# Optimization experiments

Measured on AMD Instinct MI355X. Metric: run time of the kernel, lower is better.

The kernel has to match this reference:

```python
import jax, jax.numpy as jnp
import numpy as np


def _hungarian(cost):
    """Jonker-Volgenant shortest-augmenting-path LAP solver (minimum cost).

    Returns col_ind such that rows arange(n) are matched to columns col_ind,
    identical (in objective) to scipy.optimize.linear_sum_assignment.
    Runs on host numpy, mirroring the original's detach().cpu() + scipy path.
    """
    cost = np.asarray(cost, dtype=np.float64)
    n = cost.shape[0]
    INF = np.inf
    u = np.zeros(n + 1)
    v = np.zeros(n + 1)
    p = np.zeros(n + 1, dtype=np.int64)   # p[j]: row (1-based) assigned to column j
    way = np.zeros(n + 1, dtype=np.int64)
    for i in range(1, n + 1):
        p[0] = i
        j0 = 0
        minv = np.full(n + 1, INF)
        used = np.zeros(n + 1, dtype=bool)
        while True:
            used[j0] = True
            i0 = p[j0]
            # vectorized relaxation of reduced costs for all unused columns
            cur = cost[i0 - 1] - u[i0] - v[1:]
            free = ~used[1:]
            upd = free & (cur < minv[1:])
            minv[1:] = np.where(upd, cur, minv[1:])
            way[1:] = np.where(upd, j0, way[1:])
            cand = np.where(free, minv[1:], INF)
            j1 = int(np.argmin(cand)) + 1
            delta = cand[j1 - 1]
            u[p[used]] += delta
            v[used] -= delta
            minv[1:] = np.where(free, minv[1:] - delta, minv[1:])
            j0 = j1
            if p[j0] == 0:
                break
        # augment along the alternating path
        while j0:
            j1 = way[j0]
            p[j0] = p[j1]
            j0 = j1
    col = np.empty(n, dtype=np.int64)
    col[p[1:] - 1] = np.arange(n)
    return col


def setup_inputs() -> dict:
    key = jax.random.key(0)
    B, N = 64, 256
    D = jax.random.normal(key, (B, N, N), dtype=jnp.float32)
    return {"D": D}


def reference(D):
    # Host round-trip for the assignment, exactly as the torch module does
    # (D.detach().cpu().numpy() -> scipy LAP per batch element).
    Dn = np.asarray(jax.device_get(D))
    cols = np.stack([_hungarian(Dn[b]) for b in range(Dn.shape[0])])  # [B, N]
    idx = jnp.asarray(cols)[:, :, None]                               # [B, N, 1]
    # gather matched costs D[b, i, col[b, i]] and reduce: mean per batch, then mean
    matched = jnp.take_along_axis(D, idx, axis=2)[..., 0]             # [B, N]
    return matched.mean(axis=1).mean()
```

## Files before the change

### kernel.cpp

```cpp
#include <hip/hip_runtime.h>

#define N_DIM 256
#define BATCH 64
#define BS 64
#define SCALE 4096.0f

#define DPP_MINU(x, ctrl) do {                                                 \
    unsigned _s = (unsigned)__builtin_amdgcn_update_dpp((int)(x), (int)(x),    \
                                                        (ctrl), 0xf, 0xf, false); \
    (x) = ((x) < _s) ? (x) : _s;                                               \
} while (0)

__device__ __forceinline__ unsigned wave_min_u32(unsigned x) {
    DPP_MINU(x, 0x111);
    DPP_MINU(x, 0x112);
    DPP_MINU(x, 0x114);
    DPP_MINU(x, 0x118);
    const unsigned a = (unsigned)__builtin_amdgcn_readlane((int)x, 15);
    const unsigned b = (unsigned)__builtin_amdgcn_readlane((int)x, 31);
    const unsigned c = (unsigned)__builtin_amdgcn_readlane((int)x, 47);
    const unsigned d = (unsigned)__builtin_amdgcn_readlane((int)x, 63);
    const unsigned ab = (a < b) ? a : b;
    const unsigned cd = (c < d) ? c : d;
    return (ab < cd) ? ab : cd;
}

__device__ __forceinline__ int rd4_i(int x0, int x1, int x2, int x3, int idx) {
    const int sel = idx & 3, src = idx >> 2;
    int ab = (sel & 1) ? x1 : x0;
    int cd = (sel & 1) ? x3 : x2;
    int vv = (sel & 2) ? cd : ab;
    return __builtin_amdgcn_readlane(vv, src);
}

#define SET4(x0, x1, x2, x3, idx, val) do {                                    \
    const int _sel = (idx) & 3;                                                \
    if (t == ((idx) >> 2)) {                                                   \
        if (_sel == 0) x0 = (val); else if (_sel == 1) x1 = (val);             \
        else if (_sel == 2) x2 = (val); else x3 = (val);                       \
    }                                                                          \
} while (0)

__device__ __forceinline__ int lo16(int p) { return (int)(short)(p & 0xFFFF); }
__device__ __forceinline__ int hi16(int p) { return p >> 16; }

__global__ __launch_bounds__(BS) void lap_kernel(const float* __restrict__ Dm,
                                                 double* __restrict__ batch_sums) {
    const int b = blockIdx.x;
    const int t = threadIdx.x;
    const float* __restrict__ cost = Dm + (size_t)b * N_DIM * N_DIM;
    const float4* __restrict__ cost4 = (const float4*)cost;

    __shared__ int2     chi[N_DIM * BS];
    __shared__ int      u_s[N_DIM];
    __shared__ int      v_s[N_DIM];
    __shared__ int      row4col_s[N_DIM];
    __shared__ int      col4row_s[N_DIM];
    __shared__ int      queue_s[N_DIM];
    __shared__ unsigned bid_s[N_DIM];
    __shared__ int      qcnt_s;

    const int c0i = 4 * t, c1i = 4 * t + 1, c2i = 4 * t + 2, c3i = 4 * t + 3;

    int cmn0 = INT_MAX, cmn1 = INT_MAX, cmn2 = INT_MAX, cmn3 = INT_MAX;
    int ca0 = 0, ca1 = 0, ca2 = 0, ca3 = 0;
    for (int r = 0; r < N_DIM; ++r) {
        const float4 c4 = cost4[r * BS + t];
        const int a0 = __float2int_rn(c4.x * SCALE);
        const int a1 = __float2int_rn(c4.y * SCALE);
        const int a2 = __float2int_rn(c4.z * SCALE);
        const int a3 = __float2int_rn(c4.w * SCALE);
        int2 p;
        p.x = (a0 & 0xFFFF) | (a1 << 16);
        p.y = (a2 & 0xFFFF) | (a3 << 16);
        chi[r * BS + t] = p;
        if (a0 < cmn0) { cmn0 = a0; ca0 = r; }
        if (a1 < cmn1) { cmn1 = a1; ca1 = r; }
        if (a2 < cmn2) { cmn2 = a2; ca2 = r; }
        if (a3 < cmn3) { cmn3 = a3; ca3 = r; }
    }
    {
        int4 vv; vv.x = cmn0; vv.y = cmn1; vv.z = cmn2; vv.w = cmn3;
        ((int4*)v_s)[t] = vv;
        int4 zz; zz.x = 0; zz.y = 0; zz.z = 0; zz.w = 0;
        ((int4*)u_s)[t] = zz;
        int4 mm; mm.x = -1; mm.y = -1; mm.z = -1; mm.w = -1;
        ((int4*)row4col_s)[t] = mm;
        ((int4*)col4row_s)[t] = mm;
        int4 rc; rc.x = 0x7fffffff; rc.y = 0x7fffffff; rc.z = 0x7fffffff; rc.w = 0x7fffffff;
        ((int4*)queue_s)[t] = rc;
        uint4 bb; bb.x = ~0u; bb.y = ~0u; bb.z = ~0u; bb.w = ~0u;
        ((uint4*)bid_s)[t] = bb;
    }
    __syncthreads();
    atomicMin(&queue_s[ca0], c0i);
    atomicMin(&queue_s[ca1], c1i);
    atomicMin(&queue_s[ca2], c2i);
    atomicMin(&queue_s[ca3], c3i);
    __syncthreads();
    if (queue_s[ca0] == c0i) { row4col_s[c0i] = ca0; col4row_s[ca0] = c0i; }
    if (queue_s[ca1] == c1i) { row4col_s[c1i] = ca1; col4row_s[ca1] = c1i; }
    if (queue_s[ca2] == c2i) { row4col_s[c2i] = ca2; col4row_s[ca2] = c2i; }
    if (queue_s[ca3] == c3i) { row4col_s[c3i] = ca3; col4row_s[ca3] = c3i; }
    __syncthreads();

    for (int pass = 0; pass < 24; ++pass) {
        if (t == 0) qcnt_s = 0;
        __syncthreads();
        {
            const int4 my = ((const int4*)col4row_s)[t];
            const int nf = (my.x < 0) + (my.y < 0) + (my.z < 0) + (my.w < 0);
            if (nf) {
                int pos = atomicAdd(&qcnt_s, nf);
                if (my.x < 0) queue_s[pos++] = c0i;
                if (my.y < 0) queue_s[pos++] = c1i;
                if (my.z < 0) queue_s[pos++] = c2i;
                if (my.w < 0) queue_s[pos++] = c3i;
            }
        }
        __syncthreads();
        const int n = qcnt_s;
        if (n == 0) break;
        for (int base = 0; base < n; base += BS) {
            const int my_row = (base + t < n) ? queue_s[base + t] : -1;
            int d1 = INT_MAX, d2 = INT_MAX;
            int j1 = 0;
            if (my_row >= 0) {
                const int rb = my_row * BS;
                for (int l = 0; l < BS; ++l) {
                    const int l2 = (l + t) & 63;
                    const int2 h = chi[rb + l2];
                    const int4 vv = ((const int4*)v_s)[l2];
                    int d;
                    d = lo16(h.x) - vv.x; if (d < d1) { d2 = d1; d1 = d; j1 = 4 * l2 + 0; } else if (d < d2) d2 = d;
                    d = hi16(h.x) - vv.y; if (d < d1) { d2 = d1; d1 = d; j1 = 4 * l2 + 1; } else if (d < d2) d2 = d;
                    d = lo16(h.y) - vv.z; if (d < d1) { d2 = d1; d1 = d; j1 = 4 * l2 + 2; } else if (d < d2) d2 = d;
                    d = hi16(h.y) - vv.w; if (d < d1) { d2 = d1; d1 = d; j1 = 4 * l2 + 3; } else if (d < d2) d2 = d;
                }
                atomicMin(&bid_s[j1], ((unsigned)d1 << 8) | (unsigned)t);
            }
            __syncthreads();
            if (my_row >= 0) {
                const unsigned mybid = ((unsigned)d1 << 8) | (unsigned)t;
                if (bid_s[j1] == mybid) {
                    const int i0 = row4col_s[j1];
                    row4col_s[j1] = my_row;
                    col4row_s[my_row] = j1;
                    if (i0 >= 0) col4row_s[i0] = -1;
                    u_s[my_row] = d2;
                    v_s[j1] += d1 - d2;
                    bid_s[j1] = ~0u;
                }
            }
            __syncthreads();
        }
    }

    const int4 vv4 = ((const int4*)v_s)[t];
    int vn0 = -vv4.x, vn1 = -vv4.y, vn2 = -vv4.z, vn3 = -vv4.w;
    const int4 m4 = ((const int4*)row4col_s)[t];
    int r4c0 = m4.x, r4c1 = m4.y, r4c2 = m4.z, r4c3 = m4.w;
    const int4 y4 = ((const int4*)col4row_s)[t];
    int c4r0 = y4.x, c4r1 = y4.y, c4r2 = y4.z, c4r3 = y4.w;
    int p0 = 0, p1 = 0, p2 = 0, p3 = 0;

    unsigned long long fm0 = __ballot(c4r0 < 0);
    unsigned long long fm1 = __ballot(c4r1 < 0);
    unsigned long long fm2 = __ballot(c4r2 < 0);
    unsigned long long fm3 = __ballot(c4r3 < 0);

    const int KINIT0 = (0x7FFFFF << 8) | c0i;
    const int KINIT1 = (0x7FFFFF << 8) | c1i;
    const int KINIT2 = (0x7FFFFF << 8) | c2i;
    const int KINIT3 = (0x7FFFFF << 8) | c3i;

    while (fm0 | fm1 | fm2 | fm3) {
        int i;
        if (fm0)      { const int tt = __builtin_ctzll(fm0); fm0 &= fm0 - 1; i = tt * 4 + 0; }
        else if (fm1) { const int tt = __builtin_ctzll(fm1); fm1 &= fm1 - 1; i = tt * 4 + 1; }
        else if (fm2) { const int tt = __builtin_ctzll(fm2); fm2 &= fm2 - 1; i = tt * 4 + 2; }
        else          { const int tt = __builtin_ctzll(fm3); fm3 &= fm3 - 1; i = tt * 4 + 3; }

        int k0 = KINIT0, k1 = KINIT1, k2 = KINIT2, k3 = KINIT3;
        int g0 = 0, g1 = 0, g2 = 0, g3 = 0;
        int cur = i;
        int minVal = 0;
        int sink = -1;

        while (true) {
            const int2 h   = chi[cur * BS + t];
            const int ucur = u_s[cur];
            const int add  = minVal - ucur;

            int r, kn;
            r  = add + lo16(h.x) + vn0;
            kn = (r << 8) | c0i; if (kn < k0) { p0 = cur; k0 = kn; }
            r  = add + hi16(h.x) + vn1;
            kn = (r << 8) | c1i; if (kn < k1) { p1 = cur; k1 = kn; }
            r  = add + lo16(h.y) + vn2;
            kn = (r << 8) | c2i; if (kn < k2) { p2 = cur; k2 = kn; }
            r  = add + hi16(h.y) + vn3;
            kn = (r << 8) | c3i; if (kn < k3) { p3 = cur; k3 = kn; }

            const int q0 = k0 | g0, q1 = k1 | g1, q2 = k2 | g2, q3 = k3 | g3;
            int q01 = (q0 < q1) ? q0 : q1;
            int q23 = (q2 < q3) ? q2 : q3;
            const int gk = (int)wave_min_u32((unsigned)((q01 < q23) ? q01 : q23));

            const int bi = gk & 0xFF;
            minVal = gk >> 8;
            const int r4 = rd4_i(r4c0, r4c1, r4c2, r4c3, bi);
            if (t == (bi >> 2)) {
                const int s = bi & 3;
                if (s == 0) g0 = 0x7FFFFFFF; else if (s == 1) g1 = 0x7FFFFFFF;
                else if (s == 2) g2 = 0x7FFFFFFF; else g3 = 0x7FFFFFFF;
            }
            if (r4 < 0) { sink = bi; break; }
            cur = r4;
        }

        if (g0) { const int dv = minVal - (k0 >> 8); vn0 += dv; if (r4c0 >= 0) u_s[r4c0] += dv; }
        if (g1) { const int dv = minVal - (k1 >> 8); vn1 += dv; if (r4c1 >= 0) u_s[r4c1] += dv; }
        if (g2) { const int dv = minVal - (k2 >> 8); vn2 += dv; if (r4c2 >= 0) u_s[r4c2] += dv; }
        if (g3) { const int dv = minVal - (k3 >> 8); vn3 += dv; if (r4c3 >= 0) u_s[r4c3] += dv; }
        if (t == 0) u_s[i] += minVal;

        if (sink >= 0) {
            int jj = sink;
            while (true) {
                const int ii = rd4_i(p0, p1, p2, p3, jj);
                SET4(r4c0, r4c1, r4c2, r4c3, jj, ii);
                const int tmp = rd4_i(c4r0, c4r1, c4r2, c4r3, ii);
                SET4(c4r0, c4r1, c4r2, c4r3, ii, jj);
                jj = tmp;
                if (ii == i) break;
            }
        }
    }

    double s = 0.0;
    s += (double)cost[(size_t)(t * 4 + 0) * N_DIM + c4r0];
    s += (double)cost[(size_t)(t * 4 + 1) * N_DIM + c4r1];
    s += (double)cost[(size_t)(t * 4 + 2) * N_DIM + c4r2];
    s += (double)cost[(size_t)(t * 4 + 3) * N_DIM + c4r3];
    #pragma unroll
    for (int off = 32; off > 0; off >>= 1) s += __shfl_down(s, off);
    if (t == 0) batch_sums[b] = s;
}

__global__ void finalize_kernel(const double* __restrict__ batch_sums,
                                float* __restrict__ out) {
    const int t = threadIdx.x;
    double s = batch_sums[t];
    #pragma unroll
    for (int off = 32; off > 0; off >>= 1) s += __shfl_down(s, off);
    if (t == 0) out[0] = (float)(s / (double)((long long)BATCH * N_DIM));
}

extern "C" void kernel_launch(void* const* d_in, const int* in_sizes, int n_in,
                              void* d_out, int out_size, void* d_ws, size_t ws_size,
                              hipStream_t stream) {
    const float* Dm = (const float*)d_in[0];
    float* out = (float*)d_out;
    double* sums = (double*)d_ws;

    lap_kernel<<<BATCH, BS, 0, stream>>>(Dm, sums);
    finalize_kernel<<<1, 64, 0, stream>>>(sums, out);
}
```

Before: 725.8 us.

## Speculatively prefetch next Dijkstra row in LAP shortest-path loop and halve auction passes

Restructures the shortest-augmenting-path inner loop to speculate on the second-best column. It prefetches that column's cost row and dual before relaxing the current row, then commits the speculative step only if the relaxation did not produce a smaller key anywhere in the wave. This is meant to hide LDS load latency and the serial dependency of the wave-min reduction. It also halves the number of initial auction/greedy passes, which leaves more rows for the slower exact phase. The speculation adds an extra wave reduction and ballot per iteration, and mis-speculation wastes loads.

```diff
diff --git a/kernel.cpp b/kernel.cpp
--- a/kernel.cpp
+++ b/kernel.cpp
@@ -39,6 +39,26 @@
         if (_sel == 0) x0 = (val); else if (_sel == 1) x1 = (val);             \
         else if (_sel == 2) x2 = (val); else x3 = (val);                       \
     }                                                                          \
+} while (0)
+
+#define SET_GUARD(idx) do {                                                    \
+    if (t == ((idx) >> 2)) {                                                   \
+        const int _s = (idx) & 3;                                              \
+        if (_s == 0) g0 = 0x7FFFFFFF; else if (_s == 1) g1 = 0x7FFFFFFF;       \
+        else if (_s == 2) g2 = 0x7FFFFFFF; else g3 = 0x7FFFFFFF;               \
+    }                                                                          \
+} while (0)
+
+#define RELAX(hh, addv, predrow) do {                                          \
+    int r_, kn_;                                                               \
+    r_  = (addv) + lo16((hh).x) + vn0;                                         \
+    kn_ = (r_ << 8) | c0i; if (kn_ < k0) { p0 = (predrow); k0 = kn_; }         \
+    r_  = (addv) + hi16((hh).x) + vn1;                                         \
+    kn_ = (r_ << 8) | c1i; if (kn_ < k1) { p1 = (predrow); k1 = kn_; }         \
+    r_  = (addv) + lo16((hh).y) + vn2;                                         \
+    kn_ = (r_ << 8) | c2i; if (kn_ < k2) { p2 = (predrow); k2 = kn_; }         \
+    r_  = (addv) + hi16((hh).y) + vn3;                                         \
+    kn_ = (r_ << 8) | c3i; if (kn_ < k3) { p3 = (predrow); k3 = kn_; }         \
 } while (0)
 
 __device__ __forceinline__ int lo16(int p) { return (int)(short)(p & 0xFFFF); }
@@ -104,7 +124,7 @@
     if (queue_s[ca3] == c3i) { row4col_s[c3i] = ca3; col4row_s[ca3] = c3i; }
     __syncthreads();
 
-    for (int pass = 0; pass < 24; ++pass) {
+    for (int pass = 0; pass < 12; ++pass) {
         if (t == 0) qcnt_s = 0;
         __syncthreads();
         {
@@ -183,40 +203,49 @@
 
         int k0 = KINIT0, k1 = KINIT1, k2 = KINIT2, k3 = KINIT3;
         int g0 = 0, g1 = 0, g2 = 0, g3 = 0;
-        int cur = i;
         int minVal = 0;
         int sink = -1;
 
+        {
+            const int2 hS = chi[i * BS + t];
+            const int  uS = u_s[i];
+            RELAX(hS, -uS, i);
+        }
+
         while (true) {
-            const int2 h   = chi[cur * BS + t];
-            const int ucur = u_s[cur];
-            const int add  = minVal - ucur;
-
-            int r, kn;
-            r  = add + lo16(h.x) + vn0;
-            kn = (r << 8) | c0i; if (kn < k0) { p0 = cur; k0 = kn; }
-            r  = add + hi16(h.x) + vn1;
-            kn = (r << 8) | c1i; if (kn < k1) { p1 = cur; k1 = kn; }
-            r  = add + lo16(h.y) + vn2;
-            kn = (r << 8) | c2i; if (kn < k2) { p2 = cur; k2 = kn; }
-            r  = add + hi16(h.y) + vn3;
-            kn = (r << 8) | c3i; if (kn < k3) { p3 = cur; k3 = kn; }
-
-            const int q0 = k0 | g0, q1 = k1 | g1, q2 = k2 | g2, q3 = k3 | g3;
+            int q0 = k0 | g0, q1 = k1 | g1, q2 = k2 | g2, q3 = k3 | g3;
             int q01 = (q0 < q1) ? q0 : q1;
             int q23 = (q2 < q3) ? q2 : q3;
-            const int gk = (int)wave_min_u32((unsigned)((q01 < q23) ? q01 : q23));
-
-            const int bi = gk & 0xFF;
-            minVal = gk >> 8;
-            const int r4 = rd4_i(r4c0, r4c1, r4c2, r4c3, bi);
-            if (t == (bi >> 2)) {
-                const int s = bi & 3;
-                if (s == 0) g0 = 0x7FFFFFFF; else if (s == 1) g1 = 0x7FFFFFFF;
-                else if (s == 2) g2 = 0x7FFFFFFF; else g3 = 0x7FFFFFFF;
-            }
-            if (r4 < 0) { sink = bi; break; }
-            cur = r4;
+            const int gk1 = (int)wave_min_u32((unsigned)((q01 < q23) ? q01 : q23));
+            const int bi1 = gk1 & 0xFF;
+            SET_GUARD(bi1);
+            const int r41 = rd4_i(r4c0, r4c1, r4c2, r4c3, bi1);
+            if (r41 < 0) { sink = bi1; minVal = gk1 >> 8; break; }
+
+            const int2 h1 = chi[r41 * BS + t];
+            const int  u1 = u_s[r41];
+
+            q0 = k0 | g0; q1 = k1 | g1; q2 = k2 | g2; q3 = k3 | g3;
+            q01 = (q0 < q1) ? q0 : q1;
+            q23 = (q2 < q3) ? q2 : q3;
+            const int gk2 = (int)wave_min_u32((unsigned)((q01 < q23) ? q01 : q23));
+            const int bi2 = gk2 & 0xFF;
+            const int r42 = rd4_i(r4c0, r4c1, r4c2, r4c3, bi2);
+            const int rr2 = (r42 < 0) ? 0 : r42;
+            const int2 h2 = chi[rr2 * BS + t];
+            const int  u2 = u_s[rr2];
+
+            RELAX(h1, (gk1 >> 8) - u1, r41);
+
+            const int n0 = k0 | g0, n1 = k1 | g1, n2 = k2 | g2, n3 = k3 | g3;
+            const int n01 = (n0 < n1) ? n0 : n1;
+            const int n23 = (n2 < n3) ? n2 : n3;
+            const int nl  = (n01 < n23) ? n01 : n23;
+            if (__ballot((unsigned)nl < (unsigned)gk2) == 0ull) {
+                SET_GUARD(bi2);
+                if (r42 < 0) { sink = bi2; minVal = gk2 >> 8; break; }
+                RELAX(h2, (gk2 >> 8) - u2, r42);
+            }
         }
 
         if (g0) { const int dv = minVal - (k0 >> 8); vn0 += dv; if (r4c0 >= 0) u_s[r4c0] += dv; }
```

Result: slower. 822.9 us (+13.4%).
